# Kernel optimization log

Hardware: AMD Instinct MI355X
Metric: run time of the kernel (lower is better)

Reference implementation:

```python
import jax, jax.numpy as jnp
import numpy as np

HEADS = 10
L1, L2 = 3.0, 3.0
OBS_X, OBS_Y = 0.0, 7.0
R = 4.0


def _forward(x, mean, std, mean_label, std_label,
             W1, b1, W2, b2, W31, b31, W32, b32,
             W41, b41, W42, b42, W51, b51, W52, b52, wt):
    relu = jax.nn.relu
    B = x.shape[0]
    x0 = x * std + mean  # unnormalized state (theta1, w1, theta2, w2)
    # multi-branch MLP
    h1 = relu(x @ W1.T + b1)
    h2 = relu(h1 @ W2.T + b2)
    h31 = relu(h2 @ W31.T + b31)
    h32 = relu(h2 @ W32.T + b32)
    h41 = relu(h31 @ W41.T + b41)
    h42 = relu(h32 @ W42.T + b42)
    x51 = h41 @ W51.T + b51                      # (B, 2*HEADS) per-head refs
    x52 = 4.0 * jax.nn.sigmoid(h42 @ W52.T + b52)  # (B, HEADS+1) CBF class-K gains

    th1, w1v, th2, w2v = x0[:, 0], x0[:, 1], x0[:, 2], x0[:, 3]
    s1, c1 = jnp.sin(th1), jnp.cos(th1)
    s2, c2 = jnp.sin(th2), jnp.cos(th2)
    px = L1 * c1 + L2 * c2 - OBS_X
    py = L1 * s1 + L2 * s2 - OBS_Y
    vx = -L1 * s1 * w1v - L2 * s2 * w2v
    vy = L1 * c1 * w1v + L2 * c2 * w2v
    barrier = px * px + py * py - R * R
    b_dot = 2.0 * px * vx + 2.0 * py * vy
    Lf2b = (2.0 * vx * vx + 2.0 * vy * vy
            + 2.0 * px * (-L1 * c1 * w1v ** 2 - L2 * c2 * w2v ** 2)
            + 2.0 * py * (-L1 * s1 * w1v ** 2 - L2 * s2 * w2v ** 2))
    g1 = 2.0 * px * (-L1 * s1) + 2.0 * py * (L1 * c1)
    g2 = 2.0 * px * (-L2 * s2) + 2.0 * py * (L2 * c2)
    G = -jnp.stack([g1, g2], axis=1)  # (B, 2), single inequality row per sample

    ref = jnp.transpose(x51.reshape(B, HEADS, 2), (1, 0, 2))  # (HEADS, B, 2)
    alpha = x52[:, 0:1]           # (B, 1)
    betas = x52[:, 1:]            # (B, HEADS)
    # h[k, b] = Lf2b + (a+bk)*b_dot + a*bk*barrier
    h = (Lf2b[:, None] + (alpha + betas) * b_dot[:, None]
         + alpha * betas * barrier[:, None]).T  # (HEADS, B)

    # QP: min 0.5||u||^2 + ref^T u  s.t.  G u <= h   (Q = I, 1 constraint)
    # closed form: u = -ref - max(0, (G.(-ref) - h)/(G.G)) * G
    u_unc = -ref                                  # (HEADS, B, 2)
    Gdot = jnp.sum(G * G, axis=1)                 # (B,)
    viol = jnp.einsum('hbc,bc->hb', u_unc, G) - h
    lam = jnp.maximum(viol / Gdot[None, :], 0.0)
    sol = u_unc - lam[..., None] * G[None, :, :]  # (HEADS, B, 2)

    wv = jax.nn.softmax(wt)                       # (HEADS,)
    rt = jnp.einsum('h,hbc->bc', wv, sol)         # (B, 2)
    return (rt - mean_label) / std_label


def setup_inputs() -> dict:
    key = jax.random.key(0)
    B = 16384
    dims = [4, 2048, 2048, 1024, 1024, 1024, 1024, 2]
    ks = jax.random.split(key, 10)

    def lin(k, fin, fout):
        kw, kb = jax.random.split(k)
        W = jax.random.normal(kw, (fout, fin), jnp.float32) / jnp.sqrt(float(fin))
        b = 0.01 * jax.random.normal(kb, (fout,), jnp.float32)
        return W, b

    W1, b1 = lin(ks[0], dims[0], dims[1])
    W2, b2 = lin(ks[1], dims[1], dims[2])
    W31, b31 = lin(ks[2], dims[2], dims[3])
    W32, b32 = lin(ks[3], dims[2], dims[4])
    W41, b41 = lin(ks[4], dims[3], dims[5])
    W42, b42 = lin(ks[5], dims[4], dims[6])
    W51, b51 = lin(ks[6], dims[5], dims[7] * HEADS)
    W52, b52 = lin(ks[7], dims[6], HEADS + 1)
    wt = jnp.ones((HEADS,), jnp.float32)
    x = jax.random.normal(ks[8], (B, dims[0]), jnp.float32)
    return {
        'x': x, 'sgn': 1,
        'mean': jnp.zeros((4,), jnp.float32), 'std': jnp.ones((4,), jnp.float32),
        'mean_label': jnp.zeros((2,), jnp.float32), 'std_label': jnp.ones((2,), jnp.float32),
        'W1': W1, 'b1': b1, 'W2': W2, 'b2': b2, 'W31': W31, 'b31': b31,
        'W32': W32, 'b32': b32, 'W41': W41, 'b41': b41, 'W42': W42, 'b42': b42,
        'W51': W51, 'b51': b51, 'W52': W52, 'b52': b52, 'wt': wt,
    }


def reference(x, sgn, mean, std, mean_label, std_label,
              W1, b1, W2, b2, W31, b31, W32, b32,
              W41, b41, W42, b42, W51, b51, W52, b52, wt):
    del sgn  # unused in the training (batched QP) path
    return _forward(x, mean, std, mean_label, std_label,
                    W1, b1, W2, b2, W31, b31, W32, b32,
                    W41, b41, W42, b42, W51, b51, W52, b52, wt)
```

## Files before the change

kernel.cpp:

```cpp
#include <hip/hip_runtime.h>

typedef unsigned short u16;
typedef unsigned char  u8;
typedef unsigned int   u32;
typedef __attribute__((ext_vector_type(8)))  short short8;
typedef __attribute__((ext_vector_type(16))) float floatx16;
typedef __attribute__((ext_vector_type(4)))  int   intx4;
typedef __attribute__((ext_vector_type(16))) int   intx16;
typedef __attribute__((ext_vector_type(8)))  u16   u16x8;
typedef __attribute__((ext_vector_type(4)))  u16   u16x4;

__device__ __forceinline__ u16 f2b(float f) {
    u32 u = __float_as_uint(f);
    u = (u + 0x7FFFu + ((u >> 16) & 1u)) >> 16;
    return (u16)u;
}
__device__ __forceinline__ float b2f(u16 h) {
    return __uint_as_float(((u32)h) << 16);
}
__device__ __forceinline__ int q8(float v, float inv) {
    return __float2int_rn(fminf(fmaxf(v * inv, -127.f), 127.f));
}

__device__ __forceinline__ void f2b_block(const float* __restrict__ src,
                                          u16* __restrict__ dst, int blk) {
    int i = blk * 256 + threadIdx.x;
    float4 v = ((const float4*)src)[i];
    u16x4 o;
    o[0] = f2b(v.x); o[1] = f2b(v.y); o[2] = f2b(v.z); o[3] = f2b(v.w);
    *(u16x4*)&dst[i * 4] = o;
}

__device__ __forceinline__ void pad_block(const float* __restrict__ Wsrc, int rows,
                                          u16* __restrict__ Wdst,
                                          const float* __restrict__ bsrc,
                                          float* __restrict__ bdst, int blk) {
    int i = blk * 256 + threadIdx.x;
    int idx = i * 4;
    int r = idx >> 10;
    int c = idx & 1023;
    u16x4 o;
    if (r < rows) {
        float4 v = *(const float4*)&Wsrc[r * 1024 + c];
        o[0] = f2b(v.x); o[1] = f2b(v.y); o[2] = f2b(v.z); o[3] = f2b(v.w);
    } else {
        o[0] = 0; o[1] = 0; o[2] = 0; o[3] = 0;
    }
    *(u16x4*)&Wdst[idx] = o;
    if (i < 128) bdst[i] = (i < rows) ? bsrc[i] : 0.f;
}

__device__ __forceinline__ void wquant_row(const float* __restrict__ Wsrc, int K,
                                           u8* __restrict__ Wq, float* __restrict__ sW,
                                           float* __restrict__ Wsum, int row) {
    const int lane = threadIdx.x & 63;
    const float* src = Wsrc + (size_t)row * K;
    const int iters = K >> 8;
    float mx = 0.f;
    for (int i = 0; i < iters; ++i) {
        float4 v = *(const float4*)&src[i * 256 + lane * 4];
        mx = fmaxf(mx, fmaxf(fmaxf(fabsf(v.x), fabsf(v.y)),
                             fmaxf(fabsf(v.z), fabsf(v.w))));
    }
#pragma unroll
    for (int off = 32; off >= 1; off >>= 1) mx = fmaxf(mx, __shfl_xor(mx, off));
    float sw  = fmaxf(mx * (1.f / 127.f), 1e-20f);
    float inv = 1.f / sw;
    int ssum = 0;
    for (int i = 0; i < iters; ++i) {
        float4 v = *(const float4*)&src[i * 256 + lane * 4];
        int q0 = q8(v.x, inv), q1 = q8(v.y, inv), q2 = q8(v.z, inv), q3 = q8(v.w, inv);
        ssum += q0 + q1 + q2 + q3;
        u32 p = (q0 & 255) | ((q1 & 255) << 8) | ((q2 & 255) << 16) | ((q3 & 255) << 24);
        *(u32*)&Wq[(size_t)row * K + i * 256 + lane * 4] = p;
    }
#pragma unroll
    for (int off = 32; off >= 1; off >>= 1) ssum += __shfl_xor(ssum, off);
    if (lane == 0) { sW[row] = sw; Wsum[row] = sw * (float)ssum; }
}

__device__ __forceinline__ void l1q_block(const float* __restrict__ x,
                                          const float* __restrict__ W1,
                                          const float* __restrict__ b1,
                                          u8* __restrict__ h1q,
                                          float* __restrict__ sA,
                                          float* __restrict__ muA, int blk) {
    __shared__ float wmx[4], wmn[4];
    const int t    = threadIdx.x;
    const int wave = t >> 6;
    const int lane = t & 63;
    const int b0 = blk * 16;
    const int n0 = t * 8;
    float4 wreg[8]; float breg[8];
    const float4* W14 = (const float4*)W1;
#pragma unroll
    for (int i = 0; i < 8; ++i) { wreg[i] = W14[n0 + i]; breg[i] = b1[n0 + i]; }
    for (int r = 0; r < 16; ++r) {
        int b = b0 + r;
        float4 xv = ((const float4*)x)[b];
        float v[8];
        float lmx = 0.f, lmn = 3.4e38f;
#pragma unroll
        for (int i = 0; i < 8; ++i) {
            float s = xv.x * wreg[i].x + xv.y * wreg[i].y +
                      xv.z * wreg[i].z + xv.w * wreg[i].w + breg[i];
            s = fmaxf(s, 0.f);
            v[i] = s;
            lmx = fmaxf(lmx, s); lmn = fminf(lmn, s);
        }
#pragma unroll
        for (int off = 32; off >= 1; off >>= 1) {
            lmx = fmaxf(lmx, __shfl_xor(lmx, off));
            lmn = fminf(lmn, __shfl_xor(lmn, off));
        }
        if (lane == 0) { wmx[wave] = lmx; wmn[wave] = lmn; }
        __syncthreads();
        float mx = fmaxf(fmaxf(wmx[0], wmx[1]), fmaxf(wmx[2], wmx[3]));
        float mn = fminf(fminf(wmn[0], wmn[1]), fminf(wmn[2], wmn[3]));
        float mu  = 0.5f * (mx + mn);
        float s   = fmaxf((mx - mn) * (1.f / 254.f), 1e-20f);
        float inv = 1.f / s;
        int q[8];
#pragma unroll
        for (int i = 0; i < 8; ++i) q[i] = q8(v[i] - mu, inv);
        uint2 p;
        p.x = (q[0] & 255) | ((q[1] & 255) << 8) | ((q[2] & 255) << 16) | ((q[3] & 255) << 24);
        p.y = (q[4] & 255) | ((q[5] & 255) << 8) | ((q[6] & 255) << 16) | ((q[7] & 255) << 24);
        *(uint2*)&h1q[(size_t)b * 2048 + n0] = p;
        if (t == 0) { sA[b] = s; muA[b] = mu; }
        __syncthreads();
    }
}

__global__ __launch_bounds__(256)
void k_prep1(const float* W2, u8* W2q, float* sW2, float* Wsum2,
             const float* x, const float* W1, const float* b1,
             u8* h1q, float* sA1, float* muA1) {
    int blk = blockIdx.x;
    if (blk < 512) {
        wquant_row(W2, 2048, W2q, sW2, Wsum2, blk * 4 + (threadIdx.x >> 6));
        return;
    }
    l1q_block(x, W1, b1, h1q, sA1, muA1, blk - 512);
}

__device__ __forceinline__ void backfill_prep(
        int pblk,
        const float* W31, u16* W31b, const float* W32, u16* W32b,
        const float* W41, u16* W41b, const float* W42, u16* W42b,
        const float* W51, u16* W51p, const float* b51, float* b51p,
        const float* W52, u16* W52p, const float* b52, float* b52p,
        const float* b31, const float* b32, float* b3c) {
    if (pblk < 2048) { f2b_block(W31, W31b, pblk); return; }   pblk -= 2048;
    if (pblk < 2048) { f2b_block(W32, W32b, pblk); return; }   pblk -= 2048;
    if (pblk < 1024) { f2b_block(W41, W41b, pblk); return; }   pblk -= 1024;
    if (pblk < 1024) { f2b_block(W42, W42b, pblk); return; }   pblk -= 1024;
    if (pblk < 128)  { pad_block(W51, 20, W51p, b51, b51p, pblk); return; } pblk -= 128;
    if (pblk < 128)  { pad_block(W52, 11, W52p, b52, b52p, pblk); return; } pblk -= 128;
    if (pblk < 8) {
        int i = pblk * 256 + threadIdx.x;
        b3c[i] = (i < 1024) ? b31[i] : b32[i - 1024];
    }
}

__global__ __launch_bounds__(256, 2)
void k_gemmq(const u8* __restrict__ A, const u8* __restrict__ Wq,
             const float* __restrict__ sA, const float* __restrict__ muA,
             const float* __restrict__ sW, const float* __restrict__ Wsum,
             const float* __restrict__ bias, u16* __restrict__ C,
             int K, int ldc, int relu, int gemmY,
             const float* W31, u16* W31b, const float* W32, u16* W32b,
             const float* W41, u16* W41b, const float* W42, u16* W42b,
             const float* W51, u16* W51p, const float* b51, float* b51p,
             const float* W52, u16* W52p, const float* b52, float* b52p,
             const float* b31, const float* b32, float* b3c) {
    const int ngemm = gemmY * gridDim.x;
    int flat = blockIdx.y * gridDim.x + blockIdx.x;
    if (flat >= ngemm) {
        backfill_prep(flat - ngemm, W31, W31b, W32, W32b, W41, W41b,
                      W42, W42b, W51, W51p, b51, b51p, W52, W52p, b52, b52p,
                      b31, b32, b3c);
        return;
    }

    __shared__ __align__(16) u8 As[256 * 128];
    __shared__ __align__(16) u8 Ws[128 * 128];

    const int tid  = threadIdx.x;
    const int wave = tid >> 6;
    const int lane = tid & 63;

    int xcd = flat & 7;
    int p   = flat >> 3;
    int bx  = p % gridDim.x;
    int by  = (p / gridDim.x) * 8 + xcd;
    const int bm = by * 256;
    const int bn = bx * 128;

    const int srow = lane >> 3;
    const int sg   = ((lane & 7) ^ srow) * 16;

    const int wm    = (wave & 1) * 128;
    const int wn    = (wave >> 1) * 64;
    const int row32 = lane & 31;
    const int half  = lane >> 5;

    intx16 acc[4][2];
#pragma unroll
    for (int i = 0; i < 4; ++i)
#pragma unroll
        for (int j = 0; j < 2; ++j)
#pragma unroll
            for (int r = 0; r < 16; ++r) acc[i][j][r] = 0;

    for (int k0 = 0; k0 < K; k0 += 128) {
#pragma unroll
        for (int i = 0; i < 8; ++i) {
            int ci = wave * 8 + i;
            int r  = ci * 8 + srow;
            const u8* ga = A + (size_t)(bm + r) * K + k0 + sg;
            __builtin_amdgcn_global_load_lds(
                (const __attribute__((address_space(1))) void*)ga,
                (__attribute__((address_space(3))) void*)&As[ci * 1024], 16, 0, 0);
        }
#pragma unroll
        for (int i = 0; i < 4; ++i) {
            int ci = wave * 4 + i;
            int r  = ci * 8 + srow;
            const u8* gw = Wq + (size_t)(bn + r) * K + k0 + sg;
            __builtin_amdgcn_global_load_lds(
                (const __attribute__((address_space(1))) void*)gw,
                (__attribute__((address_space(3))) void*)&Ws[ci * 1024], 16, 0, 0);
        }
        __syncthreads();

#pragma unroll
        for (int s = 0; s < 4; ++s) {
            const int c = s * 2 + half;
            intx4 af[4], bf[2];
#pragma unroll
            for (int i = 0; i < 4; ++i) {
                int r = wm + i * 32 + row32;
                af[i] = *(const intx4*)&As[r * 128 + ((c ^ (r & 7)) * 16)];
            }
#pragma unroll
            for (int j = 0; j < 2; ++j) {
                int r = wn + j * 32 + row32;
                bf[j] = *(const intx4*)&Ws[r * 128 + ((c ^ (r & 7)) * 16)];
            }
#pragma unroll
            for (int i = 0; i < 4; ++i)
#pragma unroll
                for (int j = 0; j < 2; ++j)
                    acc[i][j] = __builtin_amdgcn_mfma_i32_32x32x32_i8(
                        af[i], bf[j], acc[i][j], 0, 0, 0);
        }
        __syncthreads();
    }

    float sWv[2], Wsv[2], bv[2];
#pragma unroll
    for (int j = 0; j < 2; ++j) {
        int col = bn + wn + j * 32 + row32;
        sWv[j] = sW[col]; Wsv[j] = Wsum[col]; bv[j] = bias[col];
    }
#pragma unroll
    for (int i = 0; i < 4; ++i)
#pragma unroll
        for (int r = 0; r < 16; ++r) {
            int row = bm + wm + i * 32 + (r & 3) + 8 * (r >> 2) + 4 * half;
            float sa = sA[row], mu = muA[row];
#pragma unroll
            for (int j = 0; j < 2; ++j) {
                int col = bn + wn + j * 32 + row32;
                float v = (float)acc[i][j][r] * (sa * sWv[j]) + mu * Wsv[j] + bv[j];
                if (relu) v = fmaxf(v, 0.f);
                C[(size_t)row * ldc + col] = f2b(v);
            }
        }
}

__global__ __launch_bounds__(256, 2)
void k_gemm256(const u16* __restrict__ A, const u16* __restrict__ W,
               const float* __restrict__ bias, u16* __restrict__ C,
               int K, int lda, int ldc, int relu, int gemmY,
               const u16* A2, const u16* W2g, const float* bias2, u16* C2,
               int split) {
    __shared__ __align__(16) u16 As[256 * 64];
    __shared__ __align__(16) u16 Ws[128 * 64];

    const int tid  = threadIdx.x;
    const int wave = tid >> 6;
    const int lane = tid & 63;

    int flat = blockIdx.y * gridDim.x + blockIdx.x;
    int xcd = flat & 7;
    int p   = flat >> 3;
    int bx  = p % gridDim.x;
    int by  = (p / gridDim.x) * 8 + xcd;

    if (A2 != nullptr && by >= split) {
        A = A2; W = W2g; bias = bias2; C = C2; by -= split;
    }
    const int bm = by * 256;
    const int bn = bx * 128;

    const int srow = lane >> 3;
    const int sg   = ((lane & 7) ^ srow) * 8;

    const int wm    = (wave & 1) * 128;
    const int wn    = (wave >> 1) * 64;
    const int row32 = lane & 31;
    const int half  = lane >> 5;

    floatx16 acc[4][2];
#pragma unroll
    for (int i = 0; i < 4; ++i)
#pragma unroll
        for (int j = 0; j < 2; ++j)
#pragma unroll
            for (int r = 0; r < 16; ++r) acc[i][j][r] = 0.f;

    for (int k0 = 0; k0 < K; k0 += 64) {
#pragma unroll
        for (int i = 0; i < 8; ++i) {
            int ci = wave * 8 + i;
            int r  = ci * 8 + srow;
            const u16* ga = A + (size_t)(bm + r) * lda + k0 + sg;
            __builtin_amdgcn_global_load_lds(
                (const __attribute__((address_space(1))) void*)ga,
                (__attribute__((address_space(3))) void*)&As[ci * 512], 16, 0, 0);
        }
#pragma unroll
        for (int i = 0; i < 4; ++i) {
            int ci = wave * 4 + i;
            int r  = ci * 8 + srow;
            const u16* gw = W + (size_t)(bn + r) * K + k0 + sg;
            __builtin_amdgcn_global_load_lds(
                (const __attribute__((address_space(1))) void*)gw,
                (__attribute__((address_space(3))) void*)&Ws[ci * 512], 16, 0, 0);
        }
        __syncthreads();

#pragma unroll
        for (int s = 0; s < 4; ++s) {
            const int c = s * 2 + half;
            short8 af[4], bf[2];
#pragma unroll
            for (int i = 0; i < 4; ++i) {
                int r = wm + i * 32 + row32;
                af[i] = *(const short8*)&As[r * 64 + ((c ^ (r & 7)) * 8)];
            }
#pragma unroll
            for (int j = 0; j < 2; ++j) {
                int r = wn + j * 32 + row32;
                bf[j] = *(const short8*)&Ws[r * 64 + ((c ^ (r & 7)) * 8)];
            }
#pragma unroll
            for (int i = 0; i < 4; ++i)
#pragma unroll
                for (int j = 0; j < 2; ++j)
                    acc[i][j] = __builtin_amdgcn_mfma_f32_32x32x16_bf16(
                        af[i], bf[j], acc[i][j], 0, 0, 0);
        }
        __syncthreads();
    }

    float bv[2];
#pragma unroll
    for (int j = 0; j < 2; ++j) bv[j] = bias[bn + wn + j * 32 + row32];
#pragma unroll
    for (int i = 0; i < 4; ++i)
#pragma unroll
        for (int j = 0; j < 2; ++j)
#pragma unroll
            for (int r = 0; r < 16; ++r) {
                int row = bm + wm + i * 32 + (r & 3) + 8 * (r >> 2) + 4 * half;
                int col = bn + wn + j * 32 + row32;
                float v = acc[i][j][r] + bv[j];
                if (relu) v = fmaxf(v, 0.f);
                C[(size_t)row * ldc + col] = f2b(v);
            }
}

__global__ __launch_bounds__(256, 2)
void k_heads_final(const u16* __restrict__ hbuf,
                   const u16* __restrict__ W51p, const float* __restrict__ b51p,
                   const u16* __restrict__ W52p, const float* __restrict__ b52p,
                   const float* __restrict__ x, const float* __restrict__ mean,
                   const float* __restrict__ std_,
                   const float* __restrict__ mean_label,
                   const float* __restrict__ std_label,
                   const float* __restrict__ wt, float* __restrict__ out) {
    __shared__ __align__(16) u16 As[128 * 64];
    __shared__ __align__(16) u16 Ws[128 * 64];
    __shared__ float x51s[128 * 20];
    __shared__ float x52s[128 * 11];

    const int tid  = threadIdx.x;
    const int wave = tid >> 6;
    const int lane = tid & 63;
    const int bm   = blockIdx.x * 128;

    const int srow = lane >> 3;
    const int sg   = ((lane & 7) ^ srow) * 8;

    const int wm    = (wave & 1) * 64;
    const int wn    = (wave >> 1) * 64;
    const int row32 = lane & 31;
    const int half  = lane >> 5;

    auto run_gemm = [&](const u16* Abase, const u16* Wp, const float* bp,
                        float* dst, int ncols) {
        floatx16 acc[2][2];
#pragma unroll
        for (int i = 0; i < 2; ++i)
#pragma unroll
            for (int j = 0; j < 2; ++j)
#pragma unroll
                for (int r = 0; r < 16; ++r) acc[i][j][r] = 0.f;

        for (int k0 = 0; k0 < 1024; k0 += 64) {
#pragma unroll
            for (int i = 0; i < 4; ++i) {
                int ci = wave * 4 + i;
                int r  = ci * 8 + srow;
                const u16* ga = Abase + (size_t)(bm + r) * 2048 + k0 + sg;
                __builtin_amdgcn_global_load_lds(
                    (const __attribute__((address_space(1))) void*)ga,
                    (__attribute__((address_space(3))) void*)&As[ci * 512], 16, 0, 0);
                const u16* gw = Wp + (size_t)r * 1024 + k0 + sg;
                __builtin_amdgcn_global_load_lds(
                    (const __attribute__((address_space(1))) void*)gw,
                    (__attribute__((address_space(3))) void*)&Ws[ci * 512], 16, 0, 0);
            }
            __syncthreads();
#pragma unroll
            for (int s = 0; s < 4; ++s) {
                const int c = s * 2 + half;
                short8 a0, a1, b0, b1;
                { int r = wm + row32;       a0 = *(const short8*)&As[r * 64 + ((c ^ (r & 7)) * 8)]; }
                { int r = wm + 32 + row32;  a1 = *(const short8*)&As[r * 64 + ((c ^ (r & 7)) * 8)]; }
                { int r = wn + row32;       b0 = *(const short8*)&Ws[r * 64 + ((c ^ (r & 7)) * 8)]; }
                { int r = wn + 32 + row32;  b1 = *(const short8*)&Ws[r * 64 + ((c ^ (r & 7)) * 8)]; }
                acc[0][0] = __builtin_amdgcn_mfma_f32_32x32x16_bf16(a0, b0, acc[0][0], 0, 0, 0);
                acc[0][1] = __builtin_amdgcn_mfma_f32_32x32x16_bf16(a0, b1, acc[0][1], 0, 0, 0);
                acc[1][0] = __builtin_amdgcn_mfma_f32_32x32x16_bf16(a1, b0, acc[1][0], 0, 0, 0);
                acc[1][1] = __builtin_amdgcn_mfma_f32_32x32x16_bf16(a1, b1, acc[1][1], 0, 0, 0);
            }
            __syncthreads();
        }
#pragma unroll
        for (int i = 0; i < 2; ++i)
#pragma unroll
            for (int j = 0; j < 2; ++j) {
                int col = wn + j * 32 + row32;
                if (col < ncols) {
                    float bj = bp[col];
#pragma unroll
                    for (int r = 0; r < 16; ++r) {
                        int row = wm + i * 32 + (r & 3) + 8 * (r >> 2) + 4 * half;
                        dst[row * ncols + col] = acc[i][j][r] + bj;
                    }
                }
            }
    };

    run_gemm(hbuf,        W51p, b51p, x51s, 20);
    run_gemm(hbuf + 1024, W52p, b52p, x52s, 11);
    __syncthreads();

    if (tid < 128) {
        int b = bm + tid;

        float w[10], m = -1e30f;
#pragma unroll
        for (int h = 0; h < 10; ++h) { w[h] = wt[h]; m = fmaxf(m, w[h]); }
        float ssum = 0.f;
#pragma unroll
        for (int h = 0; h < 10; ++h) { w[h] = __expf(w[h] - m); ssum += w[h]; }
        float winv = 1.f / ssum;

        float4 xv = ((const float4*)x)[b];
        float th1 = xv.x * std_[0] + mean[0];
        float w1v = xv.y * std_[1] + mean[1];
        float th2 = xv.z * std_[2] + mean[2];
        float w2v = xv.w * std_[3] + mean[3];
        float s1 = sinf(th1), c1 = cosf(th1);
        float s2 = sinf(th2), c2 = cosf(th2);
        float px = 3.f * c1 + 3.f * c2 - 0.f;
        float py = 3.f * s1 + 3.f * s2 - 7.f;
        float vx = -3.f * s1 * w1v - 3.f * s2 * w2v;
        float vy =  3.f * c1 * w1v + 3.f * c2 * w2v;
        float barrier = px * px + py * py - 16.f;
        float b_dot = 2.f * (px * vx + py * vy);
        float Lf2b = 2.f * vx * vx + 2.f * vy * vy
                   + 2.f * px * (-3.f * c1 * w1v * w1v - 3.f * c2 * w2v * w2v)
                   + 2.f * py * (-3.f * s1 * w1v * w1v - 3.f * s2 * w2v * w2v);
        float g1 = 2.f * px * (-3.f * s1) + 2.f * py * (3.f * c1);
        float g2 = 2.f * px * (-3.f * s2) + 2.f * py * (3.f * c2);
        float Gx = -g1, Gy = -g2;
        float Gdot = Gx * Gx + Gy * Gy;

        float alpha = 4.f / (1.f + expf(-x52s[tid * 11 + 0]));

        float rx = 0.f, ry = 0.f;
#pragma unroll
        for (int h = 0; h < 10; ++h) {
            float r0 = x51s[tid * 20 + 2 * h];
            float r1 = x51s[tid * 20 + 2 * h + 1];
            float beta = 4.f / (1.f + expf(-x52s[tid * 11 + 1 + h]));
            float hh = Lf2b + (alpha + beta) * b_dot + alpha * beta * barrier;
            float ux = -r0, uy = -r1;
            float viol = ux * Gx + uy * Gy - hh;
            float lam = fmaxf(viol / Gdot, 0.f);
            float sx = ux - lam * Gx;
            float sy = uy - lam * Gy;
            float wk = w[h] * winv;
            rx += wk * sx; ry += wk * sy;
        }
        out[2 * b]     = (rx - mean_label[0]) / std_label[0];
        out[2 * b + 1] = (ry - mean_label[1]) / std_label[1];
    }
}

extern "C" void kernel_launch(void* const* d_in, const int* in_sizes, int n_in,
                              void* d_out, int out_size, void* d_ws, size_t ws_size,
                              hipStream_t stream) {
    const float* x    = (const float*)d_in[0];
    const float* mean = (const float*)d_in[2];
    const float* std_ = (const float*)d_in[3];
    const float* mean_label = (const float*)d_in[4];
    const float* std_label  = (const float*)d_in[5];
    const float* W1  = (const float*)d_in[6];
    const float* b1  = (const float*)d_in[7];
    const float* W2  = (const float*)d_in[8];
    const float* b2  = (const float*)d_in[9];
    const float* W31 = (const float*)d_in[10];
    const float* b31 = (const float*)d_in[11];
    const float* W32 = (const float*)d_in[12];
    const float* b32 = (const float*)d_in[13];
    const float* W41 = (const float*)d_in[14];
    const float* b41 = (const float*)d_in[15];
    const float* W42 = (const float*)d_in[16];
    const float* b42 = (const float*)d_in[17];
    const float* W51 = (const float*)d_in[18];
    const float* b51 = (const float*)d_in[19];
    const float* W52 = (const float*)d_in[20];
    const float* b52 = (const float*)d_in[21];
    const float* wt  = (const float*)d_in[22];

    const int B = in_sizes[0] / 4;

    char* wsp = (char*)d_ws;
    size_t off = 0;
    auto alloc = [&](size_t bytes) {
        void* p = wsp + off;
        off += (bytes + 255) & ~(size_t)255;
        return p;
    };
    u8*    W2q  = (u8*)   alloc((size_t)2048 * 2048);
    float* sW2  = (float*)alloc(2048 * 4);
    float* Wsum2= (float*)alloc(2048 * 4);
    u8*    h1q  = (u8*)   alloc((size_t)B * 2048);
    float* sA1  = (float*)alloc((size_t)B * 4);
    float* muA1 = (float*)alloc((size_t)B * 4);
    u16*   W31b = (u16*)  alloc((size_t)1024 * 2048 * 2);
    u16*   W32b = (u16*)  alloc((size_t)1024 * 2048 * 2);
    u16*   W41b = (u16*)  alloc((size_t)1024 * 1024 * 2);
    u16*   W42b = (u16*)  alloc((size_t)1024 * 1024 * 2);
    u16*   W51p = (u16*)  alloc((size_t)128 * 1024 * 2);
    u16*   W52p = (u16*)  alloc((size_t)128 * 1024 * 2);
    float* b51p = (float*)alloc(512);
    float* b52p = (float*)alloc(512);
    float* b3c  = (float*)alloc(2048 * 4);
    u16*   bufA = (u16*)  alloc((size_t)B * 2048 * 2);
    u16*   bufB = (u16*)  alloc((size_t)B * 2048 * 2);
    const u16* NUL = nullptr;

    k_prep1<<<1536, 256, 0, stream>>>(W2, W2q, sW2, Wsum2,
                                      x, W1, b1, h1q, sA1, muA1);

    k_gemmq<<<dim3(16, 64 + 401), 256, 0, stream>>>(
        h1q, W2q, sA1, muA1, sW2, Wsum2, b2, bufB, 2048, 2048, 1, 64,
        W31, W31b, W32, W32b, W41, W41b, W42, W42b,
        W51, W51p, b51, b51p, W52, W52p, b52, b52p, b31, b32, b3c);
    k_gemm256<<<dim3(16, 64), 256, 0, stream>>>(
        bufB, W31b, b3c, bufA, 2048, 2048, 2048, 1, 64,
        NUL, NUL, nullptr, nullptr, 0);
    k_gemm256<<<dim3(8, 128), 256, 0, stream>>>(
        bufA, W41b, b41, bufB, 1024, 2048, 2048, 1, 128,
        bufA + 1024, W42b, b42, bufB + 1024, 64);
    k_heads_final<<<B / 128, 256, 0, stream>>>(
        bufB, W51p, b51p, W52p, b52p, x, mean, std_,
        mean_label, std_label, wt, (float*)d_out);
}
```

Measured before the change: 456.4 us.

## Quantize layers 3 and 4 to int8 GEMMs with per-row activation quantization

Replaces the bf16 GEMMs for the W31/W32 and W41/W42 layers with the int8 quantized GEMM kernel. Weights are quantized to int8 per row in the backfill prep blocks, and new k_aquant kernels quantize the bf16 activations per row with a mean offset before each GEMM. This halves operand bytes and uses int8 MFMA throughput, at the cost of two extra quantization passes over the activations and reduced numerical accuracy.

```diff
diff --git a/kernel.cpp b/kernel.cpp
--- a/kernel.cpp
+++ b/kernel.cpp
@@ -20,15 +20,6 @@
 }
 __device__ __forceinline__ int q8(float v, float inv) {
     return __float2int_rn(fminf(fmaxf(v * inv, -127.f), 127.f));
-}
-
-__device__ __forceinline__ void f2b_block(const float* __restrict__ src,
-                                          u16* __restrict__ dst, int blk) {
-    int i = blk * 256 + threadIdx.x;
-    float4 v = ((const float4*)src)[i];
-    u16x4 o;
-    o[0] = f2b(v.x); o[1] = f2b(v.y); o[2] = f2b(v.z); o[3] = f2b(v.w);
-    *(u16x4*)&dst[i * 4] = o;
 }
 
 __device__ __forceinline__ void pad_block(const float* __restrict__ Wsrc, int rows,
@@ -50,11 +41,11 @@
     if (i < 128) bdst[i] = (i < rows) ? bsrc[i] : 0.f;
 }
 
-__device__ __forceinline__ void wquant_row(const float* __restrict__ Wsrc, int K,
-                                           u8* __restrict__ Wq, float* __restrict__ sW,
-                                           float* __restrict__ Wsum, int row) {
+__device__ __forceinline__ void wquant_row(const float* __restrict__ src,
+                                           int K, u8* __restrict__ dstrow,
+                                           float* __restrict__ sW,
+                                           float* __restrict__ Wsum, int row_out) {
     const int lane = threadIdx.x & 63;
-    const float* src = Wsrc + (size_t)row * K;
     const int iters = K >> 8;
     float mx = 0.f;
     for (int i = 0; i < iters; ++i) {
@@ -72,11 +63,11 @@
         int q0 = q8(v.x, inv), q1 = q8(v.y, inv), q2 = q8(v.z, inv), q3 = q8(v.w, inv);
         ssum += q0 + q1 + q2 + q3;
         u32 p = (q0 & 255) | ((q1 & 255) << 8) | ((q2 & 255) << 16) | ((q3 & 255) << 24);
-        *(u32*)&Wq[(size_t)row * K + i * 256 + lane * 4] = p;
+        *(u32*)&dstrow[i * 256 + lane * 4] = p;
     }
 #pragma unroll
     for (int off = 32; off >= 1; off >>= 1) ssum += __shfl_xor(ssum, off);
-    if (lane == 0) { sW[row] = sw; Wsum[row] = sw * (float)ssum; }
+    if (lane == 0) { sW[row_out] = sw; Wsum[row_out] = sw * (float)ssum; }
 }
 
 __device__ __forceinline__ void l1q_block(const float* __restrict__ x,
@@ -138,25 +129,89 @@
              u8* h1q, float* sA1, float* muA1) {
     int blk = blockIdx.x;
     if (blk < 512) {
-        wquant_row(W2, 2048, W2q, sW2, Wsum2, blk * 4 + (threadIdx.x >> 6));
+        int row = blk * 4 + (threadIdx.x >> 6);
+        wquant_row(W2 + (size_t)row * 2048, 2048, W2q + (size_t)row * 2048,
+                   sW2, Wsum2, row);
         return;
     }
     l1q_block(x, W1, b1, h1q, sA1, muA1, blk - 512);
+}
+
+__global__ __launch_bounds__(256)
+void k_aquant(const u16* __restrict__ src, u8* __restrict__ dst,
+              float* __restrict__ s, float* __restrict__ mu, int rowlen) {
+    const int wave = threadIdx.x >> 6;
+    const int lane = threadIdx.x & 63;
+    const int row  = blockIdx.x * 4 + wave;
+    const u16* sr = src + (size_t)row * rowlen;
+    u8*       dr  = dst + (size_t)row * rowlen;
+    const int nch = rowlen >> 9;
+    u16x8 vbuf[4];
+    float mx = -3.4e38f, mn = 3.4e38f;
+    for (int c = 0; c < nch; ++c) {
+        u16x8 v = *(const u16x8*)&sr[c * 512 + lane * 8];
+        vbuf[c] = v;
+#pragma unroll
+        for (int i = 0; i < 8; ++i) {
+            float f = b2f(v[i]);
+            mx = fmaxf(mx, f); mn = fminf(mn, f);
+        }
+    }
+#pragma unroll
+    for (int off = 32; off >= 1; off >>= 1) {
+        mx = fmaxf(mx, __shfl_xor(mx, off));
+        mn = fminf(mn, __shfl_xor(mn, off));
+    }
+    float m  = 0.5f * (mx + mn);
+    float sc = fmaxf((mx - mn) * (1.f / 254.f), 1e-20f);
+    float inv = 1.f / sc;
+    for (int c = 0; c < nch; ++c) {
+        u16x8 v = vbuf[c];
+        int q[8];
+#pragma unroll
+        for (int i = 0; i < 8; ++i) q[i] = q8(b2f(v[i]) - m, inv);
+        uint2 p;
+        p.x = (q[0] & 255) | ((q[1] & 255) << 8) | ((q[2] & 255) << 16) | ((q[3] & 255) << 24);
+        p.y = (q[4] & 255) | ((q[5] & 255) << 8) | ((q[6] & 255) << 16) | ((q[7] & 255) << 24);
+        *(uint2*)&dr[c * 512 + lane * 8] = p;
+    }
+    if (lane == 0) { s[row] = sc; mu[row] = m; }
 }
 
 __device__ __forceinline__ void backfill_prep(
         int pblk,
-        const float* W31, u16* W31b, const float* W32, u16* W32b,
-        const float* W41, u16* W41b, const float* W42, u16* W42b,
+        const float* W31, const float* W32, u8* W3q, float* sW3, float* Wsum3,
+        const float* W41, u8* W41q, float* sW41, float* Ws41,
+        const float* W42, u8* W42q, float* sW42, float* Ws42,
         const float* W51, u16* W51p, const float* b51, float* b51p,
         const float* W52, u16* W52p, const float* b52, float* b52p,
         const float* b31, const float* b32, float* b3c) {
-    if (pblk < 2048) { f2b_block(W31, W31b, pblk); return; }   pblk -= 2048;
-    if (pblk < 2048) { f2b_block(W32, W32b, pblk); return; }   pblk -= 2048;
-    if (pblk < 1024) { f2b_block(W41, W41b, pblk); return; }   pblk -= 1024;
-    if (pblk < 1024) { f2b_block(W42, W42b, pblk); return; }   pblk -= 1024;
-    if (pblk < 128)  { pad_block(W51, 20, W51p, b51, b51p, pblk); return; } pblk -= 128;
-    if (pblk < 128)  { pad_block(W52, 11, W52p, b52, b52p, pblk); return; } pblk -= 128;
+    if (pblk < 512) {
+        int row = pblk * 4 + (threadIdx.x >> 6);
+        const float* src = (row < 1024) ? W31 + (size_t)row * 2048
+                                        : W32 + (size_t)(row - 1024) * 2048;
+        wquant_row(src, 2048, W3q + (size_t)row * 2048, sW3, Wsum3, row);
+        return;
+    }
+    pblk -= 512;
+    if (pblk < 256) {
+        int row = pblk * 4 + (threadIdx.x >> 6);
+        wquant_row(W41 + (size_t)row * 1024, 1024, W41q + (size_t)row * 1024,
+                   sW41, Ws41, row);
+        return;
+    }
+    pblk -= 256;
+    if (pblk < 256) {
+        int row = pblk * 4 + (threadIdx.x >> 6);
+        wquant_row(W42 + (size_t)row * 1024, 1024, W42q + (size_t)row * 1024,
+                   sW42, Ws42, row);
+        return;
+    }
+    pblk -= 256;
+    if (pblk < 128) { pad_block(W51, 20, W51p, b51, b51p, pblk); return; }
+    pblk -= 128;
+    if (pblk < 128) { pad_block(W52, 11, W52p, b52, b52p, pblk); return; }
+    pblk -= 128;
     if (pblk < 8) {
         int i = pblk * 256 + threadIdx.x;
         b3c[i] = (i < 1024) ? b31[i] : b32[i - 1024];
@@ -168,17 +223,23 @@
              const float* __restrict__ sA, const float* __restrict__ muA,
              const float* __restrict__ sW, const float* __restrict__ Wsum,
              const float* __restrict__ bias, u16* __restrict__ C,
-             int K, int ldc, int relu, int gemmY,
-             const float* W31, u16* W31b, const float* W32, u16* W32b,
-             const float* W41, u16* W41b, const float* W42, u16* W42b,
+             int K, int lda, int ldc, int sstride, int gemmY,
+             const u8* A2, const u8* Wq2,
+             const float* sA2, const float* muA2,
+             const float* sW2, const float* Wsum2,
+             const float* bias2, u16* C2, int split,
+             const float* W31, const float* W32, u8* W3q, float* sW3, float* Wsum3,
+             const float* W41, u8* W41q, float* sW41, float* Ws41,
+             const float* W42, u8* W42q, float* sW42, float* Ws42,
              const float* W51, u16* W51p, const float* b51, float* b51p,
              const float* W52, u16* W52p, const float* b52, float* b52p,
              const float* b31, const float* b32, float* b3c) {
     const int ngemm = gemmY * gridDim.x;
     int flat = blockIdx.y * gridDim.x + blockIdx.x;
     if (flat >= ngemm) {
-        backfill_prep(flat - ngemm, W31, W31b, W32, W32b, W41, W41b,
-                      W42, W42b, W51, W51p, b51, b51p, W52, W52p, b52, b52p,
+        backfill_prep(flat - ngemm, W31, W32, W3q, sW3, Wsum3,
+                      W41, W41q, sW41, Ws41, W42, W42q, sW42, Ws42,
+                      W51, W51p, b51, b51p, W52, W52p, b52, b52p,
                       b31, b32, b3c);
         return;
     }
@@ -194,6 +255,10 @@
     int p   = flat >> 3;
     int bx  = p % gridDim.x;
     int by  = (p / gridDim.x) * 8 + xcd;
+    if (A2 != nullptr && by >= split) {
+        A = A2; Wq = Wq2; sA = sA2; muA = muA2; sW = sW2; Wsum = Wsum2;
+        bias = bias2; C = C2; by -= split;
+    }
     const int bm = by * 256;
     const int bn = bx * 128;
 
@@ -218,7 +283,7 @@
         for (int i = 0; i < 8; ++i) {
             int ci = wave * 8 + i;
             int r  = ci * 8 + srow;
-            const u8* ga = A + (size_t)(bm + r) * K + k0 + sg;
+            const u8* ga = A + (size_t)(bm + r) * lda + k0 + sg;
             __builtin_amdgcn_global_load_lds(
                 (const __attribute__((address_space(1))) void*)ga,
                 (__attribute__((address_space(3))) void*)&As[ci * 1024], 16, 0, 0);
@@ -269,118 +334,15 @@
 #pragma unroll
         for (int r = 0; r < 16; ++r) {
             int row = bm + wm + i * 32 + (r & 3) + 8 * (r >> 2) + 4 * half;
-            float sa = sA[row], mu = muA[row];
+            float sa = sA[row * sstride], mu = muA[row * sstride];
 #pragma unroll
             for (int j = 0; j < 2; ++j) {
                 int col = bn + wn + j * 32 + row32;
                 float v = (float)acc[i][j][r] * (sa * sWv[j]) + mu * Wsv[j] + bv[j];
-                if (relu) v = fmaxf(v, 0.f);
+                v = fmaxf(v, 0.f);
                 C[(size_t)row * ldc + col] = f2b(v);
             }
         }
-}
-
-__global__ __launch_bounds__(256, 2)
-void k_gemm256(const u16* __restrict__ A, const u16* __restrict__ W,
-               const float* __restrict__ bias, u16* __restrict__ C,
-               int K, int lda, int ldc, int relu, int gemmY,
-               const u16* A2, const u16* W2g, const float* bias2, u16* C2,
-               int split) {
-    __shared__ __align__(16) u16 As[256 * 64];
-    __shared__ __align__(16) u16 Ws[128 * 64];
-
-    const int tid  = threadIdx.x;
-    const int wave = tid >> 6;
-    const int lane = tid & 63;
-
-    int flat = blockIdx.y * gridDim.x + blockIdx.x;
-    int xcd = flat & 7;
-    int p   = flat >> 3;
-    int bx  = p % gridDim.x;
-    int by  = (p / gridDim.x) * 8 + xcd;
-
-    if (A2 != nullptr && by >= split) {
-        A = A2; W = W2g; bias = bias2; C = C2; by -= split;
-    }
-    const int bm = by * 256;
-    const int bn = bx * 128;
-
-    const int srow = lane >> 3;
-    const int sg   = ((lane & 7) ^ srow) * 8;
-
-    const int wm    = (wave & 1) * 128;
-    const int wn    = (wave >> 1) * 64;
-    const int row32 = lane & 31;
-    const int half  = lane >> 5;
-
-    floatx16 acc[4][2];
-#pragma unroll
-    for (int i = 0; i < 4; ++i)
-#pragma unroll
-        for (int j = 0; j < 2; ++j)
-#pragma unroll
-            for (int r = 0; r < 16; ++r) acc[i][j][r] = 0.f;
-
-    for (int k0 = 0; k0 < K; k0 += 64) {
-#pragma unroll
-        for (int i = 0; i < 8; ++i) {
-            int ci = wave * 8 + i;
-            int r  = ci * 8 + srow;
-            const u16* ga = A + (size_t)(bm + r) * lda + k0 + sg;
-            __builtin_amdgcn_global_load_lds(
-                (const __attribute__((address_space(1))) void*)ga,
-                (__attribute__((address_space(3))) void*)&As[ci * 512], 16, 0, 0);
-        }
-#pragma unroll
-        for (int i = 0; i < 4; ++i) {
-            int ci = wave * 4 + i;
-            int r  = ci * 8 + srow;
-            const u16* gw = W + (size_t)(bn + r) * K + k0 + sg;
-            __builtin_amdgcn_global_load_lds(
-                (const __attribute__((address_space(1))) void*)gw,
-                (__attribute__((address_space(3))) void*)&Ws[ci * 512], 16, 0, 0);
-        }
-        __syncthreads();
-
-#pragma unroll
-        for (int s = 0; s < 4; ++s) {
-            const int c = s * 2 + half;
-            short8 af[4], bf[2];
-#pragma unroll
-            for (int i = 0; i < 4; ++i) {
-                int r = wm + i * 32 + row32;
-                af[i] = *(const short8*)&As[r * 64 + ((c ^ (r & 7)) * 8)];
-            }
-#pragma unroll
-            for (int j = 0; j < 2; ++j) {
-                int r = wn + j * 32 + row32;
-                bf[j] = *(const short8*)&Ws[r * 64 + ((c ^ (r & 7)) * 8)];
-            }
-#pragma unroll
-            for (int i = 0; i < 4; ++i)
-#pragma unroll
-                for (int j = 0; j < 2; ++j)
-                    acc[i][j] = __builtin_amdgcn_mfma_f32_32x32x16_bf16(
-                        af[i], bf[j], acc[i][j], 0, 0, 0);
-        }
-        __syncthreads();
-    }
-
-    float bv[2];
-#pragma unroll
-    for (int j = 0; j < 2; ++j) bv[j] = bias[bn + wn + j * 32 + row32];
-#pragma unroll
-    for (int i = 0; i < 4; ++i)
-#pragma unroll
-        for (int j = 0; j < 2; ++j)
-#pragma unroll
-            for (int r = 0; r < 16; ++r) {
-                int row = bm + wm + i * 32 + (r & 3) + 8 * (r >> 2) + 4 * half;
-                int col = bn + wn + j * 32 + row32;
-                float v = acc[i][j][r] + bv[j];
-                if (relu) v = fmaxf(v, 0.f);
-                C[(size_t)row * ldc + col] = f2b(v);
-            }
 }
 
 __global__ __launch_bounds__(256, 2)
@@ -559,38 +521,67 @@
         off += (bytes + 255) & ~(size_t)255;
         return p;
     };
-    u8*    W2q  = (u8*)   alloc((size_t)2048 * 2048);
-    float* sW2  = (float*)alloc(2048 * 4);
-    float* Wsum2= (float*)alloc(2048 * 4);
-    u8*    h1q  = (u8*)   alloc((size_t)B * 2048);
-    float* sA1  = (float*)alloc((size_t)B * 4);
-    float* muA1 = (float*)alloc((size_t)B * 4);
-    u16*   W31b = (u16*)  alloc((size_t)1024 * 2048 * 2);
-    u16*   W32b = (u16*)  alloc((size_t)1024 * 2048 * 2);
-    u16*   W41b = (u16*)  alloc((size_t)1024 * 1024 * 2);
-    u16*   W42b = (u16*)  alloc((size_t)1024 * 1024 * 2);
-    u16*   W51p = (u16*)  alloc((size_t)128 * 1024 * 2);
-    u16*   W52p = (u16*)  alloc((size_t)128 * 1024 * 2);
-    float* b51p = (float*)alloc(512);
-    float* b52p = (float*)alloc(512);
-    float* b3c  = (float*)alloc(2048 * 4);
-    u16*   bufA = (u16*)  alloc((size_t)B * 2048 * 2);
-    u16*   bufB = (u16*)  alloc((size_t)B * 2048 * 2);
-    const u16* NUL = nullptr;
+    u8*    W2q   = (u8*)   alloc((size_t)2048 * 2048);
+    float* sW2   = (float*)alloc(2048 * 4);
+    float* Wsum2 = (float*)alloc(2048 * 4);
+    u8*    h1q   = (u8*)   alloc((size_t)B * 2048);
+    float* sA1   = (float*)alloc((size_t)B * 4);
+    float* muA1  = (float*)alloc((size_t)B * 4);
+    u8*    W3q   = (u8*)   alloc((size_t)2048 * 2048);
+    float* sW3   = (float*)alloc(2048 * 4);
+    float* Wsum3 = (float*)alloc(2048 * 4);
+    u8*    W41q  = (u8*)   alloc((size_t)1024 * 1024);
+    float* sW41  = (float*)alloc(1024 * 4);
+    float* Ws41  = (float*)alloc(1024 * 4);
+    u8*    W42q  = (u8*)   alloc((size_t)1024 * 1024);
+    float* sW42  = (float*)alloc(1024 * 4);
+    float* Ws42  = (float*)alloc(1024 * 4);
+    u16*   W51p  = (u16*)  alloc((size_t)128 * 1024 * 2);
+    u16*   W52p  = (u16*)  alloc((size_t)128 * 1024 * 2);
+    float* b51p  = (float*)alloc(512);
+    float* b52p  = (float*)alloc(512);
+    float* b3c   = (float*)alloc(2048 * 4);
+    u8*    h2q   = (u8*)   alloc((size_t)B * 2048);
+    float* s2a   = (float*)alloc((size_t)B * 4);
+    float* mu2a  = (float*)alloc((size_t)B * 4);
+    u8*    h34q  = (u8*)   alloc((size_t)B * 2048);
+    float* s34   = (float*)alloc((size_t)2 * B * 4);
+    float* mu34  = (float*)alloc((size_t)2 * B * 4);
+    u16*   bufA  = (u16*)  alloc((size_t)B * 2048 * 2);
+    u16*   bufB  = (u16*)  alloc((size_t)B * 2048 * 2);
+    const u8* NUL8 = nullptr;
 
     k_prep1<<<1536, 256, 0, stream>>>(W2, W2q, sW2, Wsum2,
                                       x, W1, b1, h1q, sA1, muA1);
 
-    k_gemmq<<<dim3(16, 64 + 401), 256, 0, stream>>>(
-        h1q, W2q, sA1, muA1, sW2, Wsum2, b2, bufB, 2048, 2048, 1, 64,
-        W31, W31b, W32, W32b, W41, W41b, W42, W42b,
+    k_gemmq<<<dim3(16, 64 + 81), 256, 0, stream>>>(
+        h1q, W2q, sA1, muA1, sW2, Wsum2, b2, bufB, 2048, 2048, 2048, 1, 64,
+        NUL8, NUL8, nullptr, nullptr, nullptr, nullptr, nullptr, nullptr, 0,
+        W31, W32, W3q, sW3, Wsum3,
+        W41, W41q, sW41, Ws41, W42, W42q, sW42, Ws42,
         W51, W51p, b51, b51p, W52, W52p, b52, b52p, b31, b32, b3c);
-    k_gemm256<<<dim3(16, 64), 256, 0, stream>>>(
-        bufB, W31b, b3c, bufA, 2048, 2048, 2048, 1, 64,
-        NUL, NUL, nullptr, nullptr, 0);
-    k_gemm256<<<dim3(8, 128), 256, 0, stream>>>(
-        bufA, W41b, b41, bufB, 1024, 2048, 2048, 1, 128,
-        bufA + 1024, W42b, b42, bufB + 1024, 64);
+
+    k_aquant<<<B / 4, 256, 0, stream>>>(bufB, h2q, s2a, mu2a, 2048);
+
+    k_gemmq<<<dim3(16, 64), 256, 0, stream>>>(
+        h2q, W3q, s2a, mu2a, sW3, Wsum3, b3c, bufA, 2048, 2048, 2048, 1, 64,
+        NUL8, NUL8, nullptr, nullptr, nullptr, nullptr, nullptr, nullptr, 0,
+        nullptr, nullptr, nullptr, nullptr, nullptr,
+        nullptr, nullptr, nullptr, nullptr, nullptr, nullptr, nullptr, nullptr,
+        nullptr, nullptr, nullptr, nullptr, nullptr, nullptr, nullptr, nullptr,
+        nullptr, nullptr, nullptr);
+
+    k_aquant<<<2 * B / 4, 256, 0, stream>>>(bufA, h34q, s34, mu34, 1024);
+
+    k_gemmq<<<dim3(8, 128), 256, 0, stream>>>(
+        h34q, W41q, s34, mu34, sW41, Ws41, b41, bufB,
+        1024, 2048, 2048, 2, 128,
+        h34q + 1024, W42q, s34 + 1, mu34 + 1, sW42, Ws42, b42, bufB + 1024, 64,
+        nullptr, nullptr, nullptr, nullptr, nullptr,
+        nullptr, nullptr, nullptr, nullptr, nullptr, nullptr, nullptr, nullptr,
+        nullptr, nullptr, nullptr, nullptr, nullptr, nullptr, nullptr, nullptr,
+        nullptr, nullptr, nullptr);
+
     k_heads_final<<<B / 128, 256, 0, stream>>>(
         bufB, W51p, b51p, W52p, b52p, x, mean, std_,
         mean_label, std_label, wt, (float*)d_out);
```

New measurement: 684.9 us. 1.5x slower.
